# Kernel tuning notes

Hardware: AMD Instinct MI355X
Metric: run time of the kernel (lower is better)

## Reference

```python
import jax, jax.numpy as jnp
import numpy as np

B, L, D, H = 4, 1024, 1024, 16
DH = D // H  # 64
TOPK = 32


def setup_inputs() -> dict:
    key = jax.random.key(0)
    ks = jax.random.split(key, 9)
    s = 1.0 / np.sqrt(D)
    return {
        "x": jax.random.normal(ks[0], (B, L, D), jnp.float32),
        "Wq": jax.random.normal(ks[1], (D, D), jnp.float32) * s,
        "bq": jax.random.normal(ks[2], (D,), jnp.float32) * 0.01,
        "Wk": jax.random.normal(ks[3], (D, D), jnp.float32) * s,
        "bk": jax.random.normal(ks[4], (D,), jnp.float32) * 0.01,
        "Wv": jax.random.normal(ks[5], (D, D), jnp.float32) * s,
        "bv": jax.random.normal(ks[6], (D,), jnp.float32) * 0.01,
        "Wo": jax.random.normal(ks[7], (D, D), jnp.float32) * s,
        "bo": jax.random.normal(ks[8], (D,), jnp.float32) * 0.01,
        "top_k": TOPK,
    }


def reference(x, Wq, bq, Wk, bk, Wv, bv, Wo, bo, top_k):
    b, l, _ = x.shape
    q = (x @ Wq + bq).reshape(b, l, H, DH)
    k = (x @ Wk + bk).reshape(b, l, H, DH)
    v = (x @ Wv + bv).reshape(b, l, H, DH)
    # scores: [B, i, j, h]
    scores = jnp.einsum('bihd,bjhd->bijh', q, k) / np.sqrt(DH).astype(np.float32)
    # softmax over axis 2 (j), as in the original (dim=2 of bijh)
    weights = jax.nn.softmax(scores, axis=2)
    if top_k is not None:
        # top-k along j: move j to last axis -> [B, i, h, j]
        w_t = jnp.swapaxes(weights, 2, 3)
        _, idx = jax.lax.top_k(w_t, top_k)
        mask = jnp.put_along_axis(jnp.zeros_like(w_t), idx, 1.0, axis=-1, inplace=False)
        w_t = w_t * mask
        w_t = w_t / (jnp.sum(w_t, axis=-1, keepdims=True) + 1e-8)
        weights = jnp.swapaxes(w_t, 2, 3)
    attn = jnp.einsum('bijh,bjhd->bihd', weights, v).reshape(b, l, D)
    return attn @ Wo + bo
```

## Files before the change

kernel.cpp:

```cpp
#include <hip/hip_runtime.h>
#include <math.h>

#define B_ 4
#define L_ 1024
#define D_ 1024
#define H_ 16
#define DH_ 64
#define M_ (B_*L_)

typedef _Float16 half8 __attribute__((ext_vector_type(8)));
typedef _Float16 half4 __attribute__((ext_vector_type(4)));
typedef float f32x4 __attribute__((ext_vector_type(4)));

#define MFMA16(a,b,c) __builtin_amdgcn_mfma_f32_16x16x32_f16(a, b, c, 0, 0, 0)

#define DPPF(oldv, x, ctrl, rmask) \
  __int_as_float(__builtin_amdgcn_update_dpp(__float_as_int(oldv), __float_as_int(x), ctrl, rmask, 0xf, false))

__device__ __forceinline__ float wfred_max(float x) {
  x = fmaxf(x, DPPF(-INFINITY, x, 0x111, 0xf));
  x = fmaxf(x, DPPF(-INFINITY, x, 0x112, 0xf));
  x = fmaxf(x, DPPF(-INFINITY, x, 0x114, 0xf));
  x = fmaxf(x, DPPF(-INFINITY, x, 0x118, 0xf));
  x = fmaxf(x, DPPF(-INFINITY, x, 0x142, 0xa));
  x = fmaxf(x, DPPF(-INFINITY, x, 0x143, 0xc));
  return __int_as_float(__builtin_amdgcn_readlane(__float_as_int(x), 63));
}
__device__ __forceinline__ float wfred_sum(float x) {
  x = x + DPPF(0.f, x, 0x111, 0xf);
  x = x + DPPF(0.f, x, 0x112, 0xf);
  x = x + DPPF(0.f, x, 0x114, 0xf);
  x = x + DPPF(0.f, x, 0x118, 0xf);
  x = x + DPPF(0.f, x, 0x142, 0xa);
  x = x + DPPF(0.f, x, 0x143, 0xc);
  return __int_as_float(__builtin_amdgcn_readlane(__float_as_int(x), 63));
}

__global__ __launch_bounds__(256) void split_x(const float* __restrict__ x,
                                               _Float16* __restrict__ xh,
                                               _Float16* __restrict__ xl) {
  const int i = blockIdx.x * 256 + threadIdx.x;
  float4 v = ((const float4*)x)[i];
  const float a0 = v.x * 16.f, a1 = v.y * 16.f, a2 = v.z * 16.f, a3 = v.w * 16.f;
  const _Float16 h0 = (_Float16)a0, h1 = (_Float16)a1, h2 = (_Float16)a2, h3 = (_Float16)a3;
  half4 hv, lv;
  hv[0] = h0; hv[1] = h1; hv[2] = h2; hv[3] = h3;
  lv[0] = (_Float16)(a0 - (float)h0);
  lv[1] = (_Float16)(a1 - (float)h1);
  lv[2] = (_Float16)(a2 - (float)h2);
  lv[3] = (_Float16)(a3 - (float)h3);
  ((half4*)xh)[i] = hv;
  ((half4*)xl)[i] = lv;
}

__global__ __launch_bounds__(256) void split_w4(const float* __restrict__ W0,
                                                const float* __restrict__ W1,
                                                const float* __restrict__ W2,
                                                const float* __restrict__ W3,
                                                _Float16* __restrict__ Whl_base) {
  const int z = blockIdx.z;
  const float* W = (z == 0) ? W0 : (z == 1) ? W1 : (z == 2) ? W2 : W3;
  _Float16* Wh = Whl_base + (size_t)z * 2 * (size_t)(D_ * D_);
  _Float16* Wl = Wh + (size_t)(D_ * D_);
  __shared__ float tile[64][65];
  const int t = threadIdx.x;
  const int tk = blockIdx.x & 15;
  const int tn = blockIdx.x >> 4;
  const int kr = t >> 2, ns = (t & 3) * 16;
  const float* src = W + (size_t)(tk * 64 + kr) * D_ + tn * 64 + ns;
  float4 v0 = ((const float4*)src)[0];
  float4 v1 = ((const float4*)src)[1];
  float4 v2 = ((const float4*)src)[2];
  float4 v3 = ((const float4*)src)[3];
  tile[ns + 0][kr] = v0.x;  tile[ns + 1][kr] = v0.y;  tile[ns + 2][kr] = v0.z;  tile[ns + 3][kr] = v0.w;
  tile[ns + 4][kr] = v1.x;  tile[ns + 5][kr] = v1.y;  tile[ns + 6][kr] = v1.z;  tile[ns + 7][kr] = v1.w;
  tile[ns + 8][kr] = v2.x;  tile[ns + 9][kr] = v2.y;  tile[ns + 10][kr] = v2.z; tile[ns + 11][kr] = v2.w;
  tile[ns + 12][kr] = v3.x; tile[ns + 13][kr] = v3.y; tile[ns + 14][kr] = v3.z; tile[ns + 15][kr] = v3.w;
  __syncthreads();
  const int nr = t >> 2, ks = (t & 3) * 16;
  const float* tr = &tile[nr][ks];
  half8 hv0, hv1, lv0, lv1;
#pragma unroll
  for (int i = 0; i < 8; i++) {
    const float s0 = tr[i] * 512.f;
    const float s1 = tr[i + 8] * 512.f;
    const _Float16 h0 = (_Float16)s0, h1 = (_Float16)s1;
    hv0[i] = h0; hv1[i] = h1;
    lv0[i] = (_Float16)(s0 - (float)h0);
    lv1[i] = (_Float16)(s1 - (float)h1);
  }
  _Float16* dh = Wh + (size_t)(tn * 64 + nr) * D_ + tk * 64 + ks;
  _Float16* dl = Wl + (size_t)(tn * 64 + nr) * D_ + tk * 64 + ks;
  *(half8*)dh = hv0; *(half8*)(dh + 8) = hv1;
  *(half8*)dl = lv0; *(half8*)(dl + 8) = lv1;
}

__device__ __forceinline__ void gemm_f16x3_body(
    const _Float16* __restrict__ Ah, const _Float16* __restrict__ Al,
    const _Float16* __restrict__ Bh, const _Float16* __restrict__ Bl,
    const float* __restrict__ bias, float* __restrict__ Cf,
    _Float16* __restrict__ Ch, _Float16* __restrict__ Cl, const bool f16out) {
  __shared__ __align__(16) _Float16 sA[2][2][128][32];
  __shared__ __align__(16) _Float16 sB[2][2][128][32];
  const int t = threadIdx.x;
  const int lane = t & 63;
  const int wid = t >> 6;
  const int bm = blockIdx.y * 128;
  const int bn = blockIdx.x * 128;

  const int m0 = t >> 2, sp0 = t & 3;
  const int sl0 = sp0 ^ ((m0 >> 1) & 3);
  const int m1 = m0 + 64;
  const _Float16* gA0h = Ah + (size_t)(bm + m0) * D_ + sl0 * 8;
  const _Float16* gA1h = Ah + (size_t)(bm + m1) * D_ + sl0 * 8;
  const _Float16* gA0l = Al + (size_t)(bm + m0) * D_ + sl0 * 8;
  const _Float16* gA1l = Al + (size_t)(bm + m1) * D_ + sl0 * 8;
  const _Float16* gB0h = Bh + (size_t)(bn + m0) * D_ + sl0 * 8;
  const _Float16* gB1h = Bh + (size_t)(bn + m1) * D_ + sl0 * 8;
  const _Float16* gB0l = Bl + (size_t)(bn + m0) * D_ + sl0 * 8;
  const _Float16* gB1l = Bl + (size_t)(bn + m1) * D_ + sl0 * 8;

  half8 rA0h = *(const half8*)(gA0h);
  half8 rA1h = *(const half8*)(gA1h);
  half8 rA0l = *(const half8*)(gA0l);
  half8 rA1l = *(const half8*)(gA1l);
  half8 rB0h = *(const half8*)(gB0h);
  half8 rB1h = *(const half8*)(gB1h);
  half8 rB0l = *(const half8*)(gB0l);
  half8 rB1l = *(const half8*)(gB1l);
  *(half8*)&sA[0][0][m0][sp0 * 8] = rA0h;
  *(half8*)&sA[0][0][m1][sp0 * 8] = rA1h;
  *(half8*)&sA[0][1][m0][sp0 * 8] = rA0l;
  *(half8*)&sA[0][1][m1][sp0 * 8] = rA1l;
  *(half8*)&sB[0][0][m0][sp0 * 8] = rB0h;
  *(half8*)&sB[0][0][m1][sp0 * 8] = rB1h;
  *(half8*)&sB[0][1][m0][sp0 * 8] = rB0l;
  *(half8*)&sB[0][1][m1][sp0 * 8] = rB1l;
  __syncthreads();

  f32x4 acc[4][4];
#pragma unroll
  for (int i = 0; i < 4; i++)
#pragma unroll
    for (int j = 0; j < 4; j++) acc[i][j] = {0.f, 0.f, 0.f, 0.f};

  const int wr = wid >> 1, wc = wid & 1;
  const int l15 = lane & 15;
  const int soff = ((lane >> 4) ^ ((l15 >> 1) & 3)) * 8;

  int p = 0;
  for (int k0 = 0; k0 < 1024; k0 += 32) {
    const bool more = (k0 + 32) < 1024;
    if (more) {
      const int kk = k0 + 32;
      rA0h = *(const half8*)(gA0h + kk);
      rA1h = *(const half8*)(gA1h + kk);
      rA0l = *(const half8*)(gA0l + kk);
      rA1l = *(const half8*)(gA1l + kk);
      rB0h = *(const half8*)(gB0h + kk);
      rB1h = *(const half8*)(gB1h + kk);
      rB0l = *(const half8*)(gB0l + kk);
      rB1l = *(const half8*)(gB1l + kk);
    }
    half8 bh[4], bl[4];
#pragma unroll
    for (int ni = 0; ni < 4; ni++) {
      const int rb = wc * 64 + ni * 16 + l15;
      bh[ni] = *(const half8*)&sB[p][0][rb][soff];
      bl[ni] = *(const half8*)&sB[p][1][rb][soff];
    }
#pragma unroll
    for (int mi = 0; mi < 4; mi++) {
      const int ra = wr * 64 + mi * 16 + l15;
      const half8 ah = *(const half8*)&sA[p][0][ra][soff];
      const half8 al = *(const half8*)&sA[p][1][ra][soff];
#pragma unroll
      for (int ni = 0; ni < 4; ni++) {
        acc[mi][ni] = MFMA16(ah, bh[ni], acc[mi][ni]);
        acc[mi][ni] = MFMA16(ah, bl[ni], acc[mi][ni]);
        acc[mi][ni] = MFMA16(al, bh[ni], acc[mi][ni]);
      }
    }
    if (more) {
      const int q = p ^ 1;
      *(half8*)&sA[q][0][m0][sp0 * 8] = rA0h;
      *(half8*)&sA[q][0][m1][sp0 * 8] = rA1h;
      *(half8*)&sA[q][1][m0][sp0 * 8] = rA0l;
      *(half8*)&sA[q][1][m1][sp0 * 8] = rA1l;
      *(half8*)&sB[q][0][m0][sp0 * 8] = rB0h;
      *(half8*)&sB[q][0][m1][sp0 * 8] = rB1h;
      *(half8*)&sB[q][1][m0][sp0 * 8] = rB0l;
      *(half8*)&sB[q][1][m1][sp0 * 8] = rB1l;
      __syncthreads();
      p = q;
    }
  }

  const float inv = 1.0f / 8192.0f;
  const int orow = bm + wr * 64 + (lane >> 4) * 4;
  const int ocol = bn + wc * 64 + l15;
#pragma unroll
  for (int ni = 0; ni < 4; ni++) {
    const int col = ocol + ni * 16;
    const float bv = bias[col];
#pragma unroll
    for (int mi = 0; mi < 4; mi++) {
      const f32x4 a = acc[mi][ni];
#pragma unroll
      for (int r = 0; r < 4; r++) {
        const size_t idx = (size_t)(orow + mi * 16 + r) * D_ + col;
        const float val = a[r] * inv + bv;
        if (f16out) {
          const float vs = val * 16.0f;
          const _Float16 hh = (_Float16)vs;
          Ch[idx] = hh;
          Cl[idx] = (_Float16)(vs - (float)hh);
        } else {
          Cf[idx] = val;
        }
      }
    }
  }
}

__global__ __launch_bounds__(256, 2) void gemm_qkv_f16(
    const _Float16* __restrict__ xh, const _Float16* __restrict__ xl,
    const _Float16* __restrict__ Whq, const _Float16* __restrict__ Wlq,
    const _Float16* __restrict__ Whk, const _Float16* __restrict__ Wlk,
    const _Float16* __restrict__ Whv, const _Float16* __restrict__ Wlv,
    const float* __restrict__ bq, const float* __restrict__ bk, const float* __restrict__ bv,
    _Float16* __restrict__ qh, _Float16* __restrict__ ql,
    _Float16* __restrict__ kh, _Float16* __restrict__ kl,
    float* __restrict__ vf) {
  const int z = blockIdx.z;
  const _Float16* Bh = (z == 0) ? Whq : (z == 1) ? Whk : Whv;
  const _Float16* Bl = (z == 0) ? Wlq : (z == 1) ? Wlk : Wlv;
  const float* bias = (z == 0) ? bq : (z == 1) ? bk : bv;
  if (z == 2) {
    gemm_f16x3_body(xh, xl, Bh, Bl, bias, vf, nullptr, nullptr, false);
  } else {
    _Float16* Ch = (z == 0) ? qh : kh;
    _Float16* Cl = (z == 0) ? ql : kl;
    gemm_f16x3_body(xh, xl, Bh, Bl, bias, nullptr, Ch, Cl, true);
  }
}

__global__ __launch_bounds__(256, 2) void gemm_out_f16(
    const _Float16* __restrict__ ah, const _Float16* __restrict__ al,
    const _Float16* __restrict__ bh, const _Float16* __restrict__ bl,
    const float* __restrict__ bias, float* __restrict__ C) {
  gemm_f16x3_body(ah, al, bh, bl, bias, C, nullptr, nullptr, false);
}

#define SSWZ(row) (((row) & 7) << 2)

__global__ __launch_bounds__(512, 4) void attn_topk_mfma(
    const _Float16* __restrict__ qh, const _Float16* __restrict__ ql,
    const _Float16* __restrict__ kh, const _Float16* __restrict__ kl,
    const float* __restrict__ vf,
    _Float16* __restrict__ awh, _Float16* __restrict__ awl) {
  __shared__ float S[8][1024];
  __shared__ int   cidx[8][64];
  __shared__ float cfe[8][64];
  const int t = threadIdx.x;
  const int lane = t & 63;
  const int w = t >> 6;
  const int id = blockIdx.x;
  const int wk = (id & 7) * 1024 + (id >> 3);
  const int it = wk & 127;
  const int bh = wk >> 7;
  const int h = bh & 15;
  const int b = bh >> 4;
  const int i0 = it * 8;
  const size_t rowbase = (size_t)b * L_;
  const int l15 = lane & 15;
  const int kgrp = lane >> 4;

  half8 Ahf[2], Alf[2];
#pragma unroll
  for (int ks = 0; ks < 2; ks++) {
    const size_t off = (rowbase + i0 + (l15 & 7)) * D_ + h * DH_ + ks * 32 + kgrp * 8;
    Ahf[ks] = *(const half8*)(qh + off);
    Alf[ks] = *(const half8*)(ql + off);
  }

  const float sscale = 1.0f / 2048.0f;
  for (int jt = 0; jt < 8; jt++) {
    const int j0 = w * 128 + jt * 16;
    const size_t koff = (rowbase + j0 + l15) * D_ + h * DH_ + kgrp * 8;
    const half8 Bh0 = *(const half8*)(kh + koff);
    const half8 Bh1 = *(const half8*)(kh + koff + 32);
    const half8 Bl0 = *(const half8*)(kl + koff);
    const half8 Bl1 = *(const half8*)(kl + koff + 32);
    f32x4 acc = {0.f, 0.f, 0.f, 0.f};
    acc = MFMA16(Ahf[0], Bh0, acc);
    acc = MFMA16(Ahf[1], Bh1, acc);
    acc = MFMA16(Ahf[0], Bl0, acc);
    acc = MFMA16(Ahf[1], Bl1, acc);
    acc = MFMA16(Alf[0], Bh0, acc);
    acc = MFMA16(Alf[1], Bh1, acc);
    if (kgrp < 2) {
      const int srow = kgrp * 4;
#pragma unroll
      for (int r = 0; r < 4; r++)
        S[srow + r][(j0 + l15) ^ SSWZ(srow + r)] = acc[r] * sscale;
    }
  }
  __syncthreads();

  const int row = w;
  const int swz = SSWZ(row);
  float sc[16];
#pragma unroll
  for (int u = 0; u < 16; u++) sc[u] = S[row][(u * 64 + lane) ^ swz];

  float mx;
  {
    float m = sc[0];
#pragma unroll
    for (int u = 1; u < 16; u++) m = fmaxf(m, sc[u]);
    mx = wfred_max(m);
  }

  float lo = mx - 16.f, hi = mx;
  for (int it2 = 0; it2 < 14; ++it2) {
    float mid = 0.5f * (lo + hi);
    int cnt = 0;
#pragma unroll
    for (int u = 0; u < 16; u++) cnt += __popcll(__ballot(sc[u] >= mid));
    if (cnt >= 32) lo = mid; else hi = mid;
  }
  int cabove = 0;
#pragma unroll
  for (int u = 0; u < 16; u++) cabove += __popcll(__ballot(sc[u] >= hi));
  float v31 = hi;
  while (cabove < 32) {
    float nx = -INFINITY;
#pragma unroll
    for (int u = 0; u < 16; u++) nx = fmaxf(nx, (sc[u] < v31) ? sc[u] : -INFINITY);
    nx = wfred_max(nx);
    int ceq = 0;
#pragma unroll
    for (int u = 0; u < 16; u++) ceq += __popcll(__ballot(sc[u] == nx));
    cabove += ceq;
    v31 = nx;
  }
  int c_eq = 0;
#pragma unroll
  for (int u = 0; u < 16; u++) c_eq += __popcll(__ballot(sc[u] == v31));
  const int c_gt = cabove - c_eq;
  const bool span = (cabove > 32);
  const int keep_eq = 32 - c_gt;
  float v32;
  if (span) {
    v32 = v31;
  } else {
    float nx = -INFINITY;
#pragma unroll
    for (int u = 0; u < 16; u++) nx = fmaxf(nx, (sc[u] < v31) ? sc[u] : -INFINITY);
    nx = wfred_max(nx);
    v32 = nx;
  }
  const float tau = 0.5f * (v31 + v32);
  const float invbeta = 166666.67f;

  float z = 0.f;
#pragma unroll
  for (int u = 0; u < 16; u++) z += __expf(sc[u] - mx);
  z = wfred_sum(z);

  bool band = false;
  if (!span) {
    int inband = 0;
#pragma unroll
    for (int u = 0; u < 16; u++)
      inband |= (fabsf(sc[u] - tau) <= 1.81e-4f) ? 1 : 0;
    band = (__ballot(inband) != 0ull);
  }

  const float cutoff = fminf(tau - 1.8e-4f, v31);
  const float* vcol = vf + rowbase * D_ + h * DH_ + lane;
  float o;
  bool fast = false;
  if (!span) {
    int run = 0;
    float psum = 0.f;
#pragma unroll
    for (int u = 0; u < 16; u++) {
      unsigned long long m = __ballot(sc[u] >= cutoff);
      if (sc[u] >= cutoff) {
        const float eu = __expf(sc[u] - mx);
        float feu;
        if (band) {
          float arg = (sc[u] - tau) * invbeta;
          float fwv = (arg > 30.f) ? 1.f : ((arg < -30.f) ? 0.f : 1.f / (1.f + __expf(-arg)));
          feu = fwv * eu;
        } else {
          feu = (sc[u] > tau) ? eu : 0.f;
        }
        int pos = run + (int)__popcll(m & ((1ull << lane) - 1ull));
        if (pos < 64) { cidx[row][pos] = u * 64 + lane; cfe[row][pos] = feu; }
        psum += feu;
      }
      run += (int)__popcll(m);
    }
    if (run <= 64) {
      fast = true;
      const float Ssum = wfred_sum(psum);
      const int npad = (run + 7) & ~7;
      if (lane < npad - run) { cidx[row][run + lane] = 0; cfe[row][run + lane] = 0.f; }
      float acc = 0.f;
      for (int c = 0; c < npad; c += 8) {
        int jx[8]; float fx[8]; float vv[8];
#pragma unroll
        for (int i = 0; i < 8; i++) { jx[i] = cidx[row][c + i]; fx[i] = cfe[row][c + i]; }
#pragma unroll
        for (int i = 0; i < 8; i++) vv[i] = vcol[(size_t)jx[i] * D_];
#pragma unroll
        for (int i = 0; i < 8; i++) acc = fmaf(fx[i], vv[i], acc);
      }
      o = acc / (Ssum + 1e-8f * z);
    }
  }
  if (!fast) {
    float Ssum = 0.f, acc = 0.f;
    int eq_seen = 0;
    for (int u = 0; u < 16; ++u) {
      unsigned long long mask = __ballot(sc[u] >= cutoff);
      while (mask) {
        int l2 = (int)__builtin_ctzll(mask);
        mask &= mask - 1;
        float s_ = __shfl(sc[u], l2, 64);
        float e_ = __expf(s_ - mx);
        float f_;
        if (span) {
          if (s_ > v31) f_ = 1.f;
          else if (s_ == v31) { f_ = (eq_seen < keep_eq) ? 1.f : 0.f; ++eq_seen; }
          else f_ = 0.f;
        } else {
          float arg = (s_ - tau) * invbeta;
          f_ = (arg > 30.f) ? 1.f : ((arg < -30.f) ? 0.f : 1.f / (1.f + __expf(-arg)));
        }
        float fe_ = f_ * e_;
        Ssum += fe_;
        acc = fmaf(fe_, vcol[(size_t)(u * 64 + l2) * D_], acc);
      }
    }
    o = acc / (Ssum + 1e-8f * z);
  }

  const float os = o * 16.0f;
  const _Float16 oh = (_Float16)os;
  const size_t oidx = (rowbase + i0 + row) * D_ + h * DH_ + lane;
  awh[oidx] = oh;
  awl[oidx] = (_Float16)(os - (float)oh);
}

extern "C" void kernel_launch(void* const* d_in, const int* in_sizes, int n_in,
                              void* d_out, int out_size, void* d_ws, size_t ws_size,
                              hipStream_t stream) {
  const float* x  = (const float*)d_in[0];
  const float* Wq = (const float*)d_in[1];
  const float* bq = (const float*)d_in[2];
  const float* Wk = (const float*)d_in[3];
  const float* bk = (const float*)d_in[4];
  const float* Wv = (const float*)d_in[5];
  const float* bv = (const float*)d_in[6];
  const float* Wo = (const float*)d_in[7];
  const float* bo = (const float*)d_in[8];
  float* out = (float*)d_out;

  const size_t MD = (size_t)M_ * D_;
  const size_t WD = (size_t)D_ * D_;
  float* slot0 = (float*)d_ws;
  float* slot1 = slot0 + MD;
  float* vf    = slot1 + MD;
  float* slot3 = vf + MD;
  float* slot4 = slot3 + MD;

  _Float16* qh = (_Float16*)slot0;  _Float16* ql = qh + MD;
  _Float16* kh = (_Float16*)slot1;  _Float16* kl = kh + MD;
  _Float16* xh = (_Float16*)slot3;  _Float16* xl = xh + MD;
  _Float16* awh = xh;
  _Float16* awl = xl;
  _Float16* Wsplit = (_Float16*)slot4;
  _Float16* Whq = Wsplit;
  _Float16* Wlq = Whq + WD;
  _Float16* Whk = Wlq + WD;
  _Float16* Wlk = Whk + WD;
  _Float16* Whv = Wlk + WD;
  _Float16* Wlv = Whv + WD;
  _Float16* Who = Wlv + WD;
  _Float16* Wlo = Who + WD;

  dim3 b256(256);
  hipLaunchKernelGGL(split_x, dim3(4096), b256, 0, stream, x, xh, xl);
  hipLaunchKernelGGL(split_w4, dim3(256, 1, 4), b256, 0, stream, Wq, Wk, Wv, Wo, Wsplit);
  hipLaunchKernelGGL(gemm_qkv_f16, dim3(8, 32, 3), b256, 0, stream,
                     xh, xl, Whq, Wlq, Whk, Wlk, Whv, Wlv, bq, bk, bv,
                     qh, ql, kh, kl, vf);
  hipLaunchKernelGGL(attn_topk_mfma, dim3(8192), dim3(512), 0, stream,
                     qh, ql, kh, kl, vf, awh, awl);
  hipLaunchKernelGGL(gemm_out_f16, dim3(8, 32), b256, 0, stream,
                     awh, awl, Who, Wlo, bo, out);
}
```

Before: 496.5 us.

## Use direct global-to-LDS loads in GEMM and software-pipeline sparse V gather

The split-fp16 GEMM now stages A/B tiles with global_load_lds, writing straight into shared memory instead of going through registers, which cuts VGPR pressure and removes explicit LDS stores. In the top-k attention kernel, the bisection iterations drop from 14 to 12, exp values are computed once and reused, and the sparse V gather is double-buffered so loads for the next chunk are issued before the FMAs on the current one. The LDS layout written by the direct loads must match the swizzled layout the old stores produced. The fewer bisection steps may also change how often the slow path is taken.

```diff
diff --git a/kernel.cpp b/kernel.cpp
--- a/kernel.cpp
+++ b/kernel.cpp
@@ -13,6 +13,13 @@
 typedef float f32x4 __attribute__((ext_vector_type(4)));
 
 #define MFMA16(a,b,c) __builtin_amdgcn_mfma_f32_16x16x32_f16(a, b, c, 0, 0, 0)
+
+__device__ __forceinline__ void glds16(const void* g, const void* s) {
+  __builtin_amdgcn_global_load_lds(
+      (const __attribute__((address_space(1))) uint32_t*)g,
+      (__attribute__((address_space(3))) uint32_t*)(uintptr_t)s,
+      16, 0, 0);
+}
 
 #define DPPF(oldv, x, ctrl, rmask) \
   __int_as_float(__builtin_amdgcn_update_dpp(__float_as_int(oldv), __float_as_int(x), ctrl, rmask, 0xf, false))
@@ -120,22 +127,22 @@
   const _Float16* gB0l = Bl + (size_t)(bn + m0) * D_ + sl0 * 8;
   const _Float16* gB1l = Bl + (size_t)(bn + m1) * D_ + sl0 * 8;
 
-  half8 rA0h = *(const half8*)(gA0h);
-  half8 rA1h = *(const half8*)(gA1h);
-  half8 rA0l = *(const half8*)(gA0l);
-  half8 rA1l = *(const half8*)(gA1l);
-  half8 rB0h = *(const half8*)(gB0h);
-  half8 rB1h = *(const half8*)(gB1h);
-  half8 rB0l = *(const half8*)(gB0l);
-  half8 rB1l = *(const half8*)(gB1l);
-  *(half8*)&sA[0][0][m0][sp0 * 8] = rA0h;
-  *(half8*)&sA[0][0][m1][sp0 * 8] = rA1h;
-  *(half8*)&sA[0][1][m0][sp0 * 8] = rA0l;
-  *(half8*)&sA[0][1][m1][sp0 * 8] = rA1l;
-  *(half8*)&sB[0][0][m0][sp0 * 8] = rB0h;
-  *(half8*)&sB[0][0][m1][sp0 * 8] = rB1h;
-  *(half8*)&sB[0][1][m0][sp0 * 8] = rB0l;
-  *(half8*)&sB[0][1][m1][sp0 * 8] = rB1l;
+  char* sAb = (char*)&sA[0][0][0][0];
+  char* sBb = (char*)&sB[0][0][0][0];
+  const int wvb = (t >> 6) * 1024;
+
+#define STAGE(pp, kk) do { \
+    glds16(gA0h + (kk), sAb + (pp) * 16384 + wvb); \
+    glds16(gA1h + (kk), sAb + (pp) * 16384 + 4096 + wvb); \
+    glds16(gA0l + (kk), sAb + (pp) * 16384 + 8192 + wvb); \
+    glds16(gA1l + (kk), sAb + (pp) * 16384 + 12288 + wvb); \
+    glds16(gB0h + (kk), sBb + (pp) * 16384 + wvb); \
+    glds16(gB1h + (kk), sBb + (pp) * 16384 + 4096 + wvb); \
+    glds16(gB0l + (kk), sBb + (pp) * 16384 + 8192 + wvb); \
+    glds16(gB1l + (kk), sBb + (pp) * 16384 + 12288 + wvb); \
+  } while (0)
+
+  STAGE(0, 0);
   __syncthreads();
 
   f32x4 acc[4][4];
@@ -151,17 +158,7 @@
   int p = 0;
   for (int k0 = 0; k0 < 1024; k0 += 32) {
     const bool more = (k0 + 32) < 1024;
-    if (more) {
-      const int kk = k0 + 32;
-      rA0h = *(const half8*)(gA0h + kk);
-      rA1h = *(const half8*)(gA1h + kk);
-      rA0l = *(const half8*)(gA0l + kk);
-      rA1l = *(const half8*)(gA1l + kk);
-      rB0h = *(const half8*)(gB0h + kk);
-      rB1h = *(const half8*)(gB1h + kk);
-      rB0l = *(const half8*)(gB0l + kk);
-      rB1l = *(const half8*)(gB1l + kk);
-    }
+    if (more) STAGE(p ^ 1, k0 + 32);
     half8 bh[4], bl[4];
 #pragma unroll
     for (int ni = 0; ni < 4; ni++) {
@@ -182,19 +179,11 @@
       }
     }
     if (more) {
-      const int q = p ^ 1;
-      *(half8*)&sA[q][0][m0][sp0 * 8] = rA0h;
-      *(half8*)&sA[q][0][m1][sp0 * 8] = rA1h;
-      *(half8*)&sA[q][1][m0][sp0 * 8] = rA0l;
-      *(half8*)&sA[q][1][m1][sp0 * 8] = rA1l;
-      *(half8*)&sB[q][0][m0][sp0 * 8] = rB0h;
-      *(half8*)&sB[q][0][m1][sp0 * 8] = rB1h;
-      *(half8*)&sB[q][1][m0][sp0 * 8] = rB0l;
-      *(half8*)&sB[q][1][m1][sp0 * 8] = rB1l;
       __syncthreads();
-      p = q;
-    }
-  }
+      p ^= 1;
+    }
+  }
+#undef STAGE
 
   const float inv = 1.0f / 8192.0f;
   const int orow = bm + wr * 64 + (lane >> 4) * 4;
@@ -323,7 +312,7 @@
   }
 
   float lo = mx - 16.f, hi = mx;
-  for (int it2 = 0; it2 < 14; ++it2) {
+  for (int it2 = 0; it2 < 12; ++it2) {
     float mid = 0.5f * (lo + hi);
     int cnt = 0;
 #pragma unroll
@@ -364,9 +353,12 @@
   const float tau = 0.5f * (v31 + v32);
   const float invbeta = 166666.67f;
 
+  float e_[16];
+#pragma unroll
+  for (int u = 0; u < 16; u++) e_[u] = __expf(sc[u] - mx);
   float z = 0.f;
 #pragma unroll
-  for (int u = 0; u < 16; u++) z += __expf(sc[u] - mx);
+  for (int u = 0; u < 16; u++) z += e_[u];
   z = wfred_sum(z);
 
   bool band = false;
@@ -389,14 +381,13 @@
     for (int u = 0; u < 16; u++) {
       unsigned long long m = __ballot(sc[u] >= cutoff);
       if (sc[u] >= cutoff) {
-        const float eu = __expf(sc[u] - mx);
         float feu;
         if (band) {
           float arg = (sc[u] - tau) * invbeta;
           float fwv = (arg > 30.f) ? 1.f : ((arg < -30.f) ? 0.f : 1.f / (1.f + __expf(-arg)));
-          feu = fwv * eu;
+          feu = fwv * e_[u];
         } else {
-          feu = (sc[u] > tau) ? eu : 0.f;
+          feu = (sc[u] > tau) ? e_[u] : 0.f;
         }
         int pos = run + (int)__popcll(m & ((1ull << lane) - 1ull));
         if (pos < 64) { cidx[row][pos] = u * 64 + lane; cfe[row][pos] = feu; }
@@ -406,20 +397,32 @@
     }
     if (run <= 64) {
       fast = true;
-      const float Ssum = wfred_sum(psum);
       const int npad = (run + 7) & ~7;
       if (lane < npad - run) { cidx[row][run + lane] = 0; cfe[row][run + lane] = 0.f; }
-      float acc = 0.f;
-      for (int c = 0; c < npad; c += 8) {
-        int jx[8]; float fx[8]; float vv[8];
-#pragma unroll
-        for (int i = 0; i < 8; i++) { jx[i] = cidx[row][c + i]; fx[i] = cfe[row][c + i]; }
-#pragma unroll
-        for (int i = 0; i < 8; i++) vv[i] = vcol[(size_t)jx[i] * D_];
-#pragma unroll
-        for (int i = 0; i < 8; i++) acc = fmaf(fx[i], vv[i], acc);
+      const int nch = npad >> 3;
+      auto ldc = [&](int c, int* J, float* F) {
+#pragma unroll
+        for (int i = 0; i < 8; i++) { J[i] = cidx[row][c * 8 + i]; F[i] = cfe[row][c * 8 + i]; }
+      };
+      auto ldv = [&](const int* J, float* V) {
+#pragma unroll
+        for (int i = 0; i < 8; i++) V[i] = vcol[(size_t)J[i] * D_];
+      };
+      auto fm8 = [&](const float* F, const float* V, float& a) {
+#pragma unroll
+        for (int i = 0; i < 8; i++) a = fmaf(F[i], V[i], a);
+      };
+      int jA[8], jB[8]; float fA[8], fB[8], vA[8], vB[8];
+      float accv = 0.f;
+      ldc(0, jA, fA); ldv(jA, vA);
+      for (int c = 0; c < nch; c += 2) {
+        if (c + 1 < nch) { ldc(c + 1, jB, fB); ldv(jB, vB); }
+        fm8(fA, vA, accv);
+        if (c + 2 < nch) { ldc(c + 2, jA, fA); ldv(jA, vA); }
+        if (c + 1 < nch) fm8(fB, vB, accv);
       }
-      o = acc / (Ssum + 1e-8f * z);
+      const float Ssum = wfred_sum(psum);
+      o = accv / (Ssum + 1e-8f * z);
     }
   }
   if (!fast) {
@@ -431,7 +434,7 @@
         int l2 = (int)__builtin_ctzll(mask);
         mask &= mask - 1;
         float s_ = __shfl(sc[u], l2, 64);
-        float e_ = __expf(s_ - mx);
+        float e2 = __expf(s_ - mx);
         float f_;
         if (span) {
           if (s_ > v31) f_ = 1.f;
@@ -441,7 +444,7 @@
           float arg = (s_ - tau) * invbeta;
           f_ = (arg > 30.f) ? 1.f : ((arg < -30.f) ? 0.f : 1.f / (1.f + __expf(-arg)));
         }
-        float fe_ = f_ * e_;
+        float fe_ = f_ * e2;
         Ssum += fe_;
         acc = fmaf(fe_, vcol[(size_t)(u * 64 + l2) * D_], acc);
       }
```

Measured after the change: 504.9 us, median of 2. Within noise of the previous version (+1.7%).
